# Kernel tuning notes

Measured on AMD Instinct MI355X. Metric: run time of the kernel, lower is better.

Reference implementation:

```python
import jax, jax.numpy as jnp
import numpy as np

N = 4096     # num nodes
FEAT = 500   # knn attribute dim
HID = 512    # args.hid_dim
E = 65536    # edges (avg degree 16)
T = 8        # args.time -> euler steps with step_size=1


def setup_inputs() -> dict:
    key = jax.random.key(0)
    ks = jax.random.split(key, 10)
    knn = jax.random.normal(ks[0], (N, FEAT), jnp.float32)
    adj = jax.random.uniform(ks[1], (N, N), jnp.float32)
    norm_factor = jnp.ones((), jnp.float32)
    edge_index = jax.random.randint(ks[2], (2, E), 0, N, dtype=jnp.int32).astype(jnp.int64)
    edge_weight = jax.random.uniform(ks[3], (E,), jnp.float32)
    # AGCN params (init eye + small noise so math is non-trivial)
    w1 = jnp.eye(N, dtype=jnp.float32) + 0.01 * jax.random.normal(ks[4], (N, N), jnp.float32)
    w2 = jnp.eye(N, dtype=jnp.float32) + 0.01 * jax.random.normal(ks[5], (N, N), jnp.float32)
    # extractor: Linear(N, HID) then Linear(HID, HID), kaiming-normal (relu), zero bias
    W0 = jax.random.normal(ks[6], (HID, N), jnp.float32) * np.float32((2.0 / N) ** 0.5)
    b0 = jnp.zeros((HID,), jnp.float32)
    W1 = jax.random.normal(ks[7], (HID, HID), jnp.float32) * np.float32((2.0 / HID) ** 0.5)
    b1 = jnp.zeros((HID,), jnp.float32)
    # LaplacianODEFunc scalar params
    alpha_train = jnp.asarray(0.5, jnp.float32)
    beta_train = jnp.asarray(0.1, jnp.float32)
    return dict(knn=knn, adj=adj, norm_factor=norm_factor, w1=w1, w2=w2,
                W0=W0, b0=b0, W1=W1, b1=b1, edge_weight=edge_weight,
                alpha_train=alpha_train, beta_train=beta_train, edge_index=edge_index)


def _spmm(edge_index, edge_weight, x):
    # out[row] += w * x[col], row=edge_index[0], col=edge_index[1]
    msg = edge_weight[:, None] * x[edge_index[1]]          # [E, HID]
    return jax.ops.segment_sum(msg, edge_index[0], num_segments=x.shape[0])


def reference(knn, adj, norm_factor, w1, w2, W0, b0, W1, b1,
              edge_weight, alpha_train, beta_train, edge_index):
    # ---- AGCN ----
    H = (adj @ w1) @ adj.T                                  # [N, N]
    H = (H @ w2) @ knn                                      # [N, FEAT]
    embed = H @ H.T                                         # [N, N]
    norm = jnp.maximum(jnp.linalg.norm(embed, axis=1, keepdims=True), 1e-12)
    embed = embed / norm                                    # F.normalize(dim=1)
    # ---- extractor MLP (no activation in source; dropout=eval no-op) ----
    h = embed @ W0.T + b0                                   # [N, HID]
    h = h @ W1.T + b1                                       # [N, HID]
    # ---- ODE diffusion: dx/dt = sigmoid(a)*(Ax - x) + b*x0, explicit Euler dt=1 ----
    x0 = jax.lax.stop_gradient(h)
    alpha = jax.nn.sigmoid(alpha_train)

    def step(x, _):
        ax = _spmm(edge_index, edge_weight, x)
        return x + alpha * (ax - x) + beta_train * x0, None

    z_ode, _ = jax.lax.scan(step, h, None, length=T)
    z = jax.nn.relu(norm_factor * z_ode + h)
    z = (z - z.mean(0)) / jnp.std(z, ddof=1)                # torch std is unbiased
    return z
```

## Files before the change

### kernel.cpp

```cpp
#include <hip/hip_runtime.h>
#include <stdint.h>
#include <stddef.h>

typedef __bf16 bf16;
typedef __attribute__((ext_vector_type(8))) __bf16 bf16x8;
typedef __attribute__((ext_vector_type(4))) __bf16 bf16x4;
typedef __attribute__((ext_vector_type(4))) float f32x4;

#define NN 4096
#define HIDD 512
#define NE 65536

__device__ inline void gll16(const void* g, void* l) {
    __builtin_amdgcn_global_load_lds(
        (const __attribute__((address_space(1))) void*)g,
        (__attribute__((address_space(3))) void*)l, 16, 0, 0);
}

__global__ void cvt8(const float* __restrict__ in, bf16* __restrict__ out, int n) {
    int i = (blockIdx.x * 256 + threadIdx.x) * 8;
    if (i >= n) return;
    float4 a = *reinterpret_cast<const float4*>(in + i);
    float4 b = *reinterpret_cast<const float4*>(in + i + 4);
    bf16x8 o;
    o[0] = (bf16)a.x; o[1] = (bf16)a.y; o[2] = (bf16)a.z; o[3] = (bf16)a.w;
    o[4] = (bf16)b.x; o[5] = (bf16)b.y; o[6] = (bf16)b.z; o[7] = (bf16)b.w;
    *reinterpret_cast<bf16x8*>(out + i) = o;
}

__global__ void reduce_bf16_slices(const bf16* __restrict__ in, bf16* __restrict__ out,
                                   int n, int S) {
    int i = (blockIdx.x * 256 + threadIdx.x) * 8;
    if (i >= n) return;
    float acc[8] = {};
    for (int k = 0; k < S; ++k) {
        bf16x8 v = *reinterpret_cast<const bf16x8*>(in + (size_t)k * n + i);
#pragma unroll
        for (int j = 0; j < 8; ++j) acc[j] += (float)v[j];
    }
    bf16x8 o;
#pragma unroll
    for (int j = 0; j < 8; ++j) o[j] = (bf16)acc[j];
    *reinterpret_cast<bf16x8*>(out + i) = o;
}

__global__ void transpose_pad_f32(const float* __restrict__ in, bf16* __restrict__ out,
                                  int R, int C, int Cpad) {
    __shared__ bf16 tile[32][33];
    int c0 = blockIdx.x * 32, r0 = blockIdx.y * 32;
    int tx = threadIdx.x, ty = threadIdx.y;
    for (int i = ty; i < 32; i += 8) {
        int r = r0 + i, c = c0 + tx;
        bf16 v = (bf16)0.f;
        if (r < R && c < C) v = (bf16)in[(size_t)r * C + c];
        tile[i][tx] = v;
    }
    __syncthreads();
    for (int i = ty; i < 32; i += 8) {
        int oc = c0 + i, orow = r0 + tx;
        if (oc < Cpad && orow < R) out[(size_t)oc * R + orow] = tile[tx][i];
    }
}

__global__ void transpose_dual_f32(const float* __restrict__ in, bf16* __restrict__ outT,
                                   bf16* __restrict__ outD, int Nn) {
    __shared__ bf16 tile[64][66];
    int r0 = blockIdx.y * 64, c0 = blockIdx.x * 64;
    int t = threadIdx.x;
    int cg = t & 7, rr = t >> 3;
#pragma unroll
    for (int i = 0; i < 2; ++i) {
        int r = rr + i * 32;
        const float* src = in + (size_t)(r0 + r) * Nn + c0 + cg * 8;
        float4 v0 = *reinterpret_cast<const float4*>(src);
        float4 v1 = *reinterpret_cast<const float4*>(src + 4);
        union { bf16x8 b; unsigned int u[4]; } cv;
        cv.b[0] = (bf16)v0.x; cv.b[1] = (bf16)v0.y; cv.b[2] = (bf16)v0.z; cv.b[3] = (bf16)v0.w;
        cv.b[4] = (bf16)v1.x; cv.b[5] = (bf16)v1.y; cv.b[6] = (bf16)v1.z; cv.b[7] = (bf16)v1.w;
        *reinterpret_cast<bf16x8*>(outD + (size_t)(r0 + r) * Nn + c0 + cg * 8) = cv.b;
        unsigned int* tw = reinterpret_cast<unsigned int*>(&tile[r][cg * 8]);
#pragma unroll
        for (int k = 0; k < 4; ++k) tw[k] = cv.u[k];
    }
    __syncthreads();
    int oc = t >> 3, rseg = (t & 7) * 8;
    bf16x8 w0, w1;
#pragma unroll
    for (int e = 0; e < 8; ++e) {
        w0[e] = tile[rseg + e][oc];
        w1[e] = tile[rseg + e][oc + 32];
    }
    *reinterpret_cast<bf16x8*>(outT + (size_t)(c0 + oc) * Nn + r0 + rseg) = w0;
    *reinterpret_cast<bf16x8*>(outT + (size_t)(c0 + oc + 32) * Nn + r0 + rseg) = w1;
}

__global__ void transpose_bf16(const bf16* __restrict__ in, bf16* __restrict__ out,
                               int R, int C) {
    __shared__ bf16 tile[32][33];
    int c0 = blockIdx.x * 32, r0 = blockIdx.y * 32;
    int tx = threadIdx.x, ty = threadIdx.y;
    for (int i = ty; i < 32; i += 8)
        tile[i][tx] = in[(size_t)(r0 + i) * C + c0 + tx];
    __syncthreads();
    for (int i = ty; i < 32; i += 8)
        out[(size_t)(c0 + i) * R + r0 + tx] = tile[tx][i];
}

template<int OMODE, bool HAS_BIAS, bool ROW_SCALE>
__global__ __launch_bounds__(256)
void gemm_nt(const bf16* __restrict__ A, const bf16* __restrict__ B,
             void* __restrict__ Cp, const float* __restrict__ bias,
             const float* __restrict__ rowscale, int M, int N, int K) {
    __shared__ __align__(16) bf16 As[3][128 * 32];
    __shared__ __align__(16) bf16 Bs[3][128 * 32];
    const int tid  = threadIdx.x;
    const int wave = tid >> 6;
    const int lane = tid & 63;
    const int m0 = blockIdx.y * 128, n0 = blockIdx.x * 128;
    const int lrow = lane >> 2;
    const int lcol = ((lane & 3) ^ ((lane >> 3) & 3)) * 8;
    const int c0 = wave * 2;
    const size_t arow0 = (size_t)(m0 + c0 * 16 + lrow) * K + lcol;
    const size_t arow1 = (size_t)(m0 + (c0 + 1) * 16 + lrow) * K + lcol;
    const size_t brow0 = (size_t)(n0 + c0 * 16 + lrow) * K + lcol;
    const size_t brow1 = (size_t)(n0 + (c0 + 1) * 16 + lrow) * K + lcol;

    f32x4 acc[4][4] = {};

    const int wm = (wave >> 1) * 64;
    const int wn = (wave & 1) * 64;
    const int fm = wm + (lane & 15);
    const int fn = wn + (lane & 15);
    const int fk = ((lane >> 4) ^ ((lane >> 1) & 3)) * 8;

    const int kper = K / gridDim.z;
    const int kz0 = blockIdx.z * kper;
    const int nt = kper >> 5;

    auto stage = [&](int t, int buf) {
        const int k0 = kz0 + (t << 5);
        gll16(A + arow0 + k0, &As[buf][c0 * 512]);
        gll16(A + arow1 + k0, &As[buf][(c0 + 1) * 512]);
        gll16(B + brow0 + k0, &Bs[buf][c0 * 512]);
        gll16(B + brow1 + k0, &Bs[buf][(c0 + 1) * 512]);
    };

    stage(0, 0);
    if (nt > 1) stage(1, 1);

    int cur = 0;
    for (int t = 0; t < nt; ++t) {
        if (t + 1 < nt) asm volatile("s_waitcnt vmcnt(4)" ::: "memory");
        else            asm volatile("s_waitcnt vmcnt(0)" ::: "memory");
        __builtin_amdgcn_s_barrier();
        if (t + 2 < nt) {
            int nb = cur + 2; if (nb >= 3) nb -= 3;
            stage(t + 2, nb);
        }
        bf16x8 af[4], bg[4];
#pragma unroll
        for (int i = 0; i < 4; ++i)
            af[i] = *reinterpret_cast<const bf16x8*>(&As[cur][(fm + i * 16) * 32 + fk]);
#pragma unroll
        for (int j = 0; j < 4; ++j)
            bg[j] = *reinterpret_cast<const bf16x8*>(&Bs[cur][(fn + j * 16) * 32 + fk]);
#pragma unroll
        for (int i = 0; i < 4; ++i)
#pragma unroll
            for (int j = 0; j < 4; ++j)
                acc[i][j] = __builtin_amdgcn_mfma_f32_16x16x32_bf16(af[i], bg[j], acc[i][j], 0, 0, 0);
        cur = (cur + 1 == 3) ? 0 : cur + 1;
    }

    const int rbase = m0 + wm + (lane >> 4) * 4;
    const int cbase = n0 + wn + (lane & 15);
    float* outf = (float*)Cp + (size_t)blockIdx.z * M * N;
    bf16*  outb = (bf16*)Cp;
    bf16*  outp = (bf16*)Cp + (size_t)blockIdx.z * M * N;
#pragma unroll
    for (int i = 0; i < 4; ++i) {
#pragma unroll
        for (int j = 0; j < 4; ++j) {
            int col = cbase + j * 16;
            float bv = 0.f;
            if (HAS_BIAS) bv = bias[col];
#pragma unroll
            for (int r = 0; r < 4; ++r) {
                int row = rbase + i * 16 + r;
                float v = acc[i][j][r];
                if (ROW_SCALE) v *= rowscale[row];
                v += bv;
                if (OMODE == 0)      outf[(size_t)row * N + col] = v;
                else if (OMODE == 1) outb[(size_t)row * N + col] = (bf16)v;
                else                 outp[(size_t)row * N + col] = (bf16)v;
            }
        }
    }
}

__global__ void colnorm_part(const bf16* __restrict__ Ht, const float* __restrict__ Rf,
                             float* __restrict__ n2) {
    int i = blockIdx.x * 128 + threadIdx.x;
    int a0 = blockIdx.y * 64;
    const size_t n = (size_t)HIDD * NN;
    float s = 0.f;
    for (int a = a0; a < a0 + 64; ++a) {
        size_t idx = (size_t)a * NN + i;
        float r = Rf[idx] + Rf[n + idx] + Rf[2 * n + idx] + Rf[3 * n + idx];
        s += r * (float)Ht[idx];
    }
    atomicAdd(&n2[i], s);
}

__global__ void bias_fuse(const float* __restrict__ W1, const float* __restrict__ b0,
                          const float* __restrict__ b1, float* __restrict__ bp) {
    int row = blockIdx.x * 4 + (threadIdx.x >> 6);
    int lane = threadIdx.x & 63;
    const float4* wr = (const float4*)(W1 + (size_t)row * HIDD);
    const float4* bz = (const float4*)b0;
    float s = 0.f;
#pragma unroll
    for (int j = 0; j < 2; ++j) {
        float4 a = wr[lane * 2 + j], b = bz[lane * 2 + j];
        s += a.x * b.x + a.y * b.y + a.z * b.z + a.w * b.w;
    }
    for (int off = 32; off; off >>= 1) s += __shfl_down(s, off);
    if (lane == 0) bp[row] = b1[row] + s;
}

__global__ void reduce4_scale_bias(const bf16* __restrict__ p, bf16* __restrict__ out,
                                   const float* __restrict__ n2, const float* __restrict__ bp) {
    int i = (blockIdx.x * 256 + threadIdx.x) * 8;
    const int n = NN * HIDD;
    float acc[8] = {};
#pragma unroll
    for (int s = 0; s < 4; ++s) {
        bf16x8 v = *reinterpret_cast<const bf16x8*>(p + (size_t)s * n + i);
#pragma unroll
        for (int j = 0; j < 8; ++j) acc[j] += (float)v[j];
    }
    int row = i >> 9;
    int col = i & (HIDD - 1);
    float sc = 1.f / fmaxf(sqrtf(n2[row]), 1e-12f);
    bf16x8 o;
#pragma unroll
    for (int j = 0; j < 8; ++j)
        o[j] = (bf16)(acc[j] * sc + bp[col + j]);
    *reinterpret_cast<bf16x8*>(out + i) = o;
}

__global__ void csr_count(const int* __restrict__ ei, int* __restrict__ cnt, int E) {
    int e = blockIdx.x * 256 + threadIdx.x;
    if (e < E) atomicAdd(&cnt[ei[e]], 1);
}

__global__ void scan_4096(const int* __restrict__ cnt, int* __restrict__ rs,
                          int* __restrict__ cur) {
    __shared__ int s[1024];
    int t = threadIdx.x;
    int b = t * 4;
    int a0 = cnt[b], a1 = cnt[b + 1], a2 = cnt[b + 2], a3 = cnt[b + 3];
    int tot = a0 + a1 + a2 + a3;
    s[t] = tot;
    __syncthreads();
    for (int off = 1; off < 1024; off <<= 1) {
        int v = (t >= off) ? s[t - off] : 0;
        __syncthreads();
        s[t] += v;
        __syncthreads();
    }
    int excl = s[t] - tot;
    rs[b] = excl; rs[b + 1] = excl + a0; rs[b + 2] = excl + a0 + a1; rs[b + 3] = excl + a0 + a1 + a2;
    cur[b] = excl; cur[b + 1] = excl + a0; cur[b + 2] = excl + a0 + a1; cur[b + 3] = excl + a0 + a1 + a2;
    if (t == 1023) rs[4096] = s[1023];
}

__global__ void csr_scatter(const int* __restrict__ ei, const float* __restrict__ ew,
                            int* __restrict__ cur, int* __restrict__ ccol,
                            float* __restrict__ cw, int E) {
    int e = blockIdx.x * 256 + threadIdx.x;
    if (e < E) {
        int r = ei[e];
        int p = atomicAdd(&cur[r], 1);
        ccol[p] = ei[E + e];
        cw[p] = ew[e];
    }
}

__global__ void ode_step_bf16(const bf16* __restrict__ xin, const bf16* __restrict__ x0,
                              bf16* __restrict__ xout, const int* __restrict__ rs,
                              const int* __restrict__ ccol, const float* __restrict__ cw,
                              const float* __restrict__ alpha_p, const float* __restrict__ beta_p) {
    int row = blockIdx.x * 4 + (threadIdx.x >> 6);
    int lane = threadIdx.x & 63;
    float alpha = 1.f / (1.f + expf(-alpha_p[0]));
    float beta = beta_p[0];
    const bf16x8* xin8 = (const bf16x8*)xin;
    float acc[8] = {};
    int p0 = rs[row], p1 = rs[row + 1];
    for (int p = p0; p < p1; ++p) {
        int c = ccol[p]; float w = cw[p];
        bf16x8 v = xin8[(size_t)c * 64 + lane];
#pragma unroll
        for (int j = 0; j < 8; ++j) acc[j] += w * (float)v[j];
    }
    bf16x8 xi = xin8[(size_t)row * 64 + lane];
    bf16x8 xz = ((const bf16x8*)x0)[(size_t)row * 64 + lane];
    bf16x8 r;
#pragma unroll
    for (int j = 0; j < 8; ++j) {
        float x = (float)xi[j];
        r[j] = (bf16)(x + alpha * (acc[j] - x) + beta * (float)xz[j]);
    }
    ((bf16x8*)xout)[(size_t)row * 64 + lane] = r;
}

__global__ void epi1(const bf16* __restrict__ x8, const bf16* __restrict__ h,
                     const float* __restrict__ nf_p,
                     float* __restrict__ colsum, float* __restrict__ gst) {
    __shared__ float r1[512], r2[512];
    int b = blockIdx.x, j = threadIdx.x;
    float nf = nf_p[0];
    float cp = 0.f, sq = 0.f;
    for (int i = 0; i < 8; ++i) {
        size_t idx = (size_t)(b * 8 + i) * HIDD + j;
        float v = nf * (float)x8[idx] + (float)h[idx];
        v = fmaxf(v, 0.f);
        cp += v; sq += v * v;
    }
    atomicAdd(&colsum[j], cp);
    r1[j] = cp; r2[j] = sq;
    __syncthreads();
    for (int off = 256; off > 0; off >>= 1) {
        if (j < off) { r1[j] += r1[j + off]; r2[j] += r2[j + off]; }
        __syncthreads();
    }
    if (j == 0) { atomicAdd(&gst[0], r1[0]); atomicAdd(&gst[1], r2[0]); }
}

__global__ void epi2(const bf16* __restrict__ x8, const bf16* __restrict__ h,
                     const float* __restrict__ nf_p, const float* __restrict__ colsum,
                     const float* __restrict__ gst, float* __restrict__ out) {
    int i = (blockIdx.x * 256 + threadIdx.x) * 8;
    float nf = nf_p[0];
    float n = (float)NN * (float)HIDD;
    float gmean = gst[0] / n;
    float var = (gst[1] - n * gmean * gmean) / (n - 1.f);
    float istd = rsqrtf(var);
    int col = i & (HIDD - 1);
    bf16x8 xv = *reinterpret_cast<const bf16x8*>(x8 + i);
    bf16x8 hv = *reinterpret_cast<const bf16x8*>(h + i);
    float4 o0, o1;
    float ov[8];
#pragma unroll
    for (int j = 0; j < 8; ++j) {
        float v = fmaxf(nf * (float)xv[j] + (float)hv[j], 0.f);
        float mean = colsum[col + j] * (1.f / (float)NN);
        ov[j] = (v - mean) * istd;
    }
    o0.x = ov[0]; o0.y = ov[1]; o0.z = ov[2]; o0.w = ov[3];
    o1.x = ov[4]; o1.y = ov[5]; o1.z = ov[6]; o1.w = ov[7];
    *reinterpret_cast<float4*>(out + i) = o0;
    *reinterpret_cast<float4*>(out + i + 4) = o1;
}

extern "C" void kernel_launch(void* const* d_in, const int* in_sizes, int n_in,
                              void* d_out, int out_size, void* d_ws, size_t ws_size,
                              hipStream_t stream) {
    const float* knn  = (const float*)d_in[0];
    const float* adj  = (const float*)d_in[1];
    const float* nf   = (const float*)d_in[2];
    const float* w1   = (const float*)d_in[3];
    const float* w2   = (const float*)d_in[4];
    const float* W0   = (const float*)d_in[5];
    const float* b0   = (const float*)d_in[6];
    const float* W1   = (const float*)d_in[7];
    const float* b1   = (const float*)d_in[8];
    const float* ew   = (const float*)d_in[9];
    const float* alph = (const float*)d_in[10];
    const float* beta = (const float*)d_in[11];
    const int*   ei   = (const int*)d_in[12];

    char* w = (char*)d_ws;
    size_t off = 0;
    auto alloc = [&](size_t bytes) -> char* {
        char* p = w + off;
        off += (bytes + 255) & ~(size_t)255;
        return p;
    };
    const size_t SZ_NN  = (size_t)NN * NN * sizeof(bf16);
    const size_t SZ_TH  = (size_t)HIDD * NN * sizeof(bf16);
    bf16* Bar  = (bf16*)alloc(SZ_NN);
    bf16* Car  = (bf16*)alloc(SZ_NN);
    bf16* Adjb = (bf16*)alloc(SZ_NN);
    bf16* W1big= (bf16*)alloc(SZ_NN);
    bf16* knnT = (bf16*)alloc(SZ_TH);
    bf16* tA   = (bf16*)alloc(SZ_TH);
    bf16* tB   = (bf16*)alloc(SZ_TH);
    float* tf  = (float*)alloc((size_t)32 * 1024 * 1024);
    bf16* Hm   = (bf16*)alloc(SZ_TH);
    bf16* W0b  = (bf16*)alloc(SZ_TH);
    bf16* W1sb = (bf16*)alloc((size_t)HIDD * HIDD * sizeof(bf16));
    bf16* Gb   = (bf16*)alloc((size_t)HIDD * HIDD * sizeof(bf16));
    bf16* M0b  = (bf16*)alloc((size_t)HIDD * HIDD * sizeof(bf16));
    bf16* Qtb  = (bf16*)alloc((size_t)HIDD * HIDD * sizeof(bf16));
    bf16* hb   = (bf16*)alloc((size_t)NN * HIDD * sizeof(bf16));
    float* n2  = (float*)alloc(NN * sizeof(float));
    int*  cnt  = (int*)alloc(NN * sizeof(int));
    int*  rs   = (int*)alloc((NN + 1) * sizeof(int));
    int*  cur  = (int*)alloc(NN * sizeof(int));
    int*  ccol = (int*)alloc(NE * sizeof(int));
    float* cw  = (float*)alloc(NE * sizeof(float));
    float* colsum = (float*)alloc(HIDD * sizeof(float));
    float* gst = (float*)alloc(2 * sizeof(float));
    float* bp  = (float*)alloc(HIDD * sizeof(float));
    bf16* tfb = (bf16*)tf;
    bf16* xA  = (bf16*)Car;
    bf16* xB  = (bf16*)Car + (size_t)NN * HIDD;
    (void)ws_size; (void)n_in; (void)in_sizes; (void)out_size;

    dim3 tb(32, 8);
    const int nTH = HIDD * NN;
    const int nHH = HIDD * HIDD;

    cvt8<<<(NN * NN) / 2048, 256, 0, stream>>>(w2, Car, NN * NN);
    cvt8<<<(NN * NN) / 2048, 256, 0, stream>>>(w1, W1big, NN * NN);
    cvt8<<<(HIDD * NN) / 2048, 256, 0, stream>>>(W0, W0b, HIDD * NN);
    cvt8<<<(HIDD * HIDD) / 2048, 256, 0, stream>>>(W1, W1sb, HIDD * HIDD);
    transpose_pad_f32<<<dim3(16, 128), tb, 0, stream>>>(knn, knnT, NN, 500, HIDD);
    transpose_dual_f32<<<dim3(64, 64), 256, 0, stream>>>(adj, Bar, Adjb, NN);

    gemm_nt<2, false, false><<<dim3(32, 4, 4), 256, 0, stream>>>(knnT, Car, tfb, nullptr, nullptr, HIDD, NN, NN);
    reduce_bf16_slices<<<nTH / 2048, 256, 0, stream>>>(tfb, tA, nTH, 4);
    gemm_nt<2, false, false><<<dim3(32, 4, 4), 256, 0, stream>>>(tA, Bar, tfb, nullptr, nullptr, HIDD, NN, NN);
    reduce_bf16_slices<<<nTH / 2048, 256, 0, stream>>>(tfb, tB, nTH, 4);
    gemm_nt<2, false, false><<<dim3(32, 4, 4), 256, 0, stream>>>(tB, W1big, tfb, nullptr, nullptr, HIDD, NN, NN);
    reduce_bf16_slices<<<nTH / 2048, 256, 0, stream>>>(tfb, tA, nTH, 4);
    gemm_nt<2, false, false><<<dim3(32, 4, 4), 256, 0, stream>>>(tA, Adjb, tfb, nullptr, nullptr, HIDD, NN, NN);
    reduce_bf16_slices<<<nTH / 2048, 256, 0, stream>>>(tfb, tB, nTH, 4);

    transpose_bf16<<<dim3(128, 16), tb, 0, stream>>>(tB, Hm, HIDD, NN);

    gemm_nt<2, false, false><<<dim3(4, 4, 32), 256, 0, stream>>>(tB, tB, tfb, nullptr, nullptr, HIDD, HIDD, NN);
    reduce_bf16_slices<<<nHH / 2048, 256, 0, stream>>>(tfb, Gb, nHH, 32);

    gemm_nt<0, false, false><<<dim3(32, 4, 4), 256, 0, stream>>>(Gb, Hm, tf, nullptr, nullptr, HIDD, NN, HIDD);
    hipMemsetAsync(n2, 0, NN * sizeof(float), stream);
    colnorm_part<<<dim3(32, 8), 128, 0, stream>>>(tB, tf, n2);

    gemm_nt<2, false, false><<<dim3(4, 4, 32), 256, 0, stream>>>(tB, W0b, tfb, nullptr, nullptr, HIDD, HIDD, NN);
    reduce_bf16_slices<<<nHH / 2048, 256, 0, stream>>>(tfb, M0b, nHH, 32);

    gemm_nt<2, false, false><<<dim3(4, 4, 8), 256, 0, stream>>>(W1sb, M0b, tfb, nullptr, nullptr, HIDD, HIDD, HIDD);
    reduce_bf16_slices<<<nHH / 2048, 256, 0, stream>>>(tfb, Qtb, nHH, 8);

    bias_fuse<<<128, 256, 0, stream>>>(W1, b0, b1, bp);

    gemm_nt<2, false, false><<<dim3(4, 32, 4), 256, 0, stream>>>(Hm, Qtb, tfb, nullptr, nullptr, NN, HIDD, HIDD);
    reduce4_scale_bias<<<(NN * HIDD) / 2048, 256, 0, stream>>>(tfb, hb, n2, bp);

    hipMemsetAsync(cnt, 0, NN * sizeof(int), stream);
    csr_count<<<NE / 256, 256, 0, stream>>>(ei, cnt, NE);
    scan_4096<<<1, 1024, 0, stream>>>(cnt, rs, cur);
    csr_scatter<<<NE / 256, 256, 0, stream>>>(ei, ew, cur, ccol, cw, NE);

    const bf16* xi = hb;
    bf16* xo = xA;
    for (int s = 0; s < 8; ++s) {
        ode_step_bf16<<<NN / 4, 256, 0, stream>>>(xi, hb, xo, rs, ccol, cw, alph, beta);
        xi = xo;
        xo = (s % 2 == 0) ? xB : xA;
    }

    hipMemsetAsync(colsum, 0, HIDD * sizeof(float), stream);
    hipMemsetAsync(gst, 0, 2 * sizeof(float), stream);
    epi1<<<NN / 8, 512, 0, stream>>>(xB, hb, nf, colsum, gst);
    epi2<<<(NN * HIDD) / 2048, 256, 0, stream>>>(xB, hb, nf, colsum, gst, (float*)d_out);
}
```

Measured before the change: 659.1 us.

## Remap GEMM blocks per XCD and halve split-K for the K=512 GEMMs

Adds an XCD-aware remapping of the flattened block index in the GEMM so blocks that are consecutive in the x/y/z order land on the same XCD, which should improve L2 reuse of the shared A/B tiles. Separately, the two K=512 GEMMs move from split-K of 4 to 2, with the colnorm and reduce kernels changed to sum two partial slices instead of four. This cuts partial-output traffic and reduction work, at the cost of fewer blocks and therefore lower occupancy in those GEMMs.

```diff
diff --git a/kernel.cpp b/kernel.cpp
--- a/kernel.cpp
+++ b/kernel.cpp
@@ -113,10 +113,21 @@
              const float* __restrict__ rowscale, int M, int N, int K) {
     __shared__ __align__(16) bf16 As[3][128 * 32];
     __shared__ __align__(16) bf16 Bs[3][128 * 32];
+    const int nx = gridDim.x, ny = gridDim.y, nz = gridDim.z;
+    const int total = nx * ny * nz;
+    int flat = blockIdx.x + nx * (blockIdx.y + ny * blockIdx.z);
+    int q = total >> 3, r8 = total & 7;
+    int xcd = flat & 7, idx = flat >> 3;
+    int swz = (xcd < r8 ? xcd * (q + 1) : r8 * (q + 1) + (xcd - r8) * q) + idx;
+    const int bx = swz / (ny * nz);
+    int rem = swz - bx * (ny * nz);
+    const int by = rem / nz;
+    const int bz = rem - by * nz;
+
     const int tid  = threadIdx.x;
     const int wave = tid >> 6;
     const int lane = tid & 63;
-    const int m0 = blockIdx.y * 128, n0 = blockIdx.x * 128;
+    const int m0 = by * 128, n0 = bx * 128;
     const int lrow = lane >> 2;
     const int lcol = ((lane & 3) ^ ((lane >> 3) & 3)) * 8;
     const int c0 = wave * 2;
@@ -133,8 +144,8 @@
     const int fn = wn + (lane & 15);
     const int fk = ((lane >> 4) ^ ((lane >> 1) & 3)) * 8;
 
-    const int kper = K / gridDim.z;
-    const int kz0 = blockIdx.z * kper;
+    const int kper = K / nz;
+    const int kz0 = bz * kper;
     const int nt = kper >> 5;
 
     auto stage = [&](int t, int buf) {
@@ -174,9 +185,9 @@
 
     const int rbase = m0 + wm + (lane >> 4) * 4;
     const int cbase = n0 + wn + (lane & 15);
-    float* outf = (float*)Cp + (size_t)blockIdx.z * M * N;
+    float* outf = (float*)Cp + (size_t)bz * M * N;
     bf16*  outb = (bf16*)Cp;
-    bf16*  outp = (bf16*)Cp + (size_t)blockIdx.z * M * N;
+    bf16*  outp = (bf16*)Cp + (size_t)bz * M * N;
 #pragma unroll
     for (int i = 0; i < 4; ++i) {
 #pragma unroll
@@ -202,12 +213,11 @@
                              float* __restrict__ n2) {
     int i = blockIdx.x * 128 + threadIdx.x;
     int a0 = blockIdx.y * 64;
-    const size_t n = (size_t)HIDD * NN;
+    const float* Rf2 = Rf + (size_t)HIDD * NN;
     float s = 0.f;
     for (int a = a0; a < a0 + 64; ++a) {
         size_t idx = (size_t)a * NN + i;
-        float r = Rf[idx] + Rf[n + idx] + Rf[2 * n + idx] + Rf[3 * n + idx];
-        s += r * (float)Ht[idx];
+        s += (Rf[idx] + Rf2[idx]) * (float)Ht[idx];
     }
     atomicAdd(&n2[i], s);
 }
@@ -228,24 +238,19 @@
     if (lane == 0) bp[row] = b1[row] + s;
 }
 
-__global__ void reduce4_scale_bias(const bf16* __restrict__ p, bf16* __restrict__ out,
+__global__ void reduce2_scale_bias(const bf16* __restrict__ p, bf16* __restrict__ out,
                                    const float* __restrict__ n2, const float* __restrict__ bp) {
     int i = (blockIdx.x * 256 + threadIdx.x) * 8;
     const int n = NN * HIDD;
-    float acc[8] = {};
-#pragma unroll
-    for (int s = 0; s < 4; ++s) {
-        bf16x8 v = *reinterpret_cast<const bf16x8*>(p + (size_t)s * n + i);
-#pragma unroll
-        for (int j = 0; j < 8; ++j) acc[j] += (float)v[j];
-    }
+    bf16x8 a = *reinterpret_cast<const bf16x8*>(p + i);
+    bf16x8 b = *reinterpret_cast<const bf16x8*>(p + n + i);
     int row = i >> 9;
     int col = i & (HIDD - 1);
     float sc = 1.f / fmaxf(sqrtf(n2[row]), 1e-12f);
     bf16x8 o;
 #pragma unroll
     for (int j = 0; j < 8; ++j)
-        o[j] = (bf16)(acc[j] * sc + bp[col + j]);
+        o[j] = (bf16)(((float)a[j] + (float)b[j]) * sc + bp[col + j]);
     *reinterpret_cast<bf16x8*>(out + i) = o;
 }
 
@@ -444,7 +449,7 @@
     gemm_nt<2, false, false><<<dim3(4, 4, 32), 256, 0, stream>>>(tB, tB, tfb, nullptr, nullptr, HIDD, HIDD, NN);
     reduce_bf16_slices<<<nHH / 2048, 256, 0, stream>>>(tfb, Gb, nHH, 32);
 
-    gemm_nt<0, false, false><<<dim3(32, 4, 4), 256, 0, stream>>>(Gb, Hm, tf, nullptr, nullptr, HIDD, NN, HIDD);
+    gemm_nt<0, false, false><<<dim3(32, 4, 2), 256, 0, stream>>>(Gb, Hm, tf, nullptr, nullptr, HIDD, NN, HIDD);
     hipMemsetAsync(n2, 0, NN * sizeof(float), stream);
     colnorm_part<<<dim3(32, 8), 128, 0, stream>>>(tB, tf, n2);
 
@@ -456,8 +461,8 @@
 
     bias_fuse<<<128, 256, 0, stream>>>(W1, b0, b1, bp);
 
-    gemm_nt<2, false, false><<<dim3(4, 32, 4), 256, 0, stream>>>(Hm, Qtb, tfb, nullptr, nullptr, NN, HIDD, HIDD);
-    reduce4_scale_bias<<<(NN * HIDD) / 2048, 256, 0, stream>>>(tfb, hb, n2, bp);
+    gemm_nt<2, false, false><<<dim3(4, 32, 2), 256, 0, stream>>>(Hm, Qtb, tfb, nullptr, nullptr, NN, HIDD, HIDD);
+    reduce2_scale_bias<<<(NN * HIDD) / 2048, 256, 0, stream>>>(tfb, hb, n2, bp);
 
     hipMemsetAsync(cnt, 0, NN * sizeof(int), stream);
     csr_count<<<NE / 256, 256, 0, stream>>>(ei, cnt, NE);
```

New measurement: 653.8 us. No clear change (-0.8%).

## Add 128x256 triple-buffered GEMM for big chain and trim split-K reductions

Applied to the files above, without the earlier changes.

Adds a new 512-thread GEMM kernel with 128x256 tiles, a three-stage LDS pipeline fed by global_load_lds and a swizzled layout. The four large 512x4096x4096 chain GEMMs use it with split-K of 8. Several smaller GEMMs drop from split-K 4 to 2, which lets the column-norm kernel run without atomics or a memset. The bias-fuse work is merged into the Q reduction kernel and the two epilogue memsets become one, cutting launch count. The risk is more split-K partial traffic in the big GEMMs and less parallelism in the shrunken splits.

```diff
diff --git a/kernel.cpp b/kernel.cpp
--- a/kernel.cpp
+++ b/kernel.cpp
@@ -198,54 +198,141 @@
     }
 }
 
-__global__ void colnorm_part(const bf16* __restrict__ Ht, const float* __restrict__ Rf,
-                             float* __restrict__ n2) {
+__global__ __launch_bounds__(512)
+void gemm_nt8(const bf16* __restrict__ A, const bf16* __restrict__ B,
+              void* __restrict__ Cp, int M, int N, int K) {
+    __shared__ __align__(16) bf16 As[3][128 * 32];
+    __shared__ __align__(16) bf16 Bs[3][256 * 32];
+    const int tid  = threadIdx.x;
+    const int wave = tid >> 6;
+    const int lane = tid & 63;
+    const int m0 = blockIdx.y * 128, n0 = blockIdx.x * 256;
+    const int lrow = lane >> 2;
+    const int lcol = ((lane & 3) ^ ((lane >> 3) & 3)) * 8;
+    const size_t arow  = (size_t)(m0 + wave * 16 + lrow) * K + lcol;
+    const size_t brow0 = (size_t)(n0 + wave * 32 + lrow) * K + lcol;
+    const size_t brow1 = (size_t)(n0 + wave * 32 + 16 + lrow) * K + lcol;
+
+    f32x4 acc[4][4] = {};
+
+    const int wm = (wave >> 2) * 64;
+    const int wn = (wave & 3) * 64;
+    const int fm = wm + (lane & 15);
+    const int fn = wn + (lane & 15);
+    const int fk = ((lane >> 4) ^ ((lane >> 1) & 3)) * 8;
+
+    const int kper = K / gridDim.z;
+    const int kz0 = blockIdx.z * kper;
+    const int nt = kper >> 5;
+
+    auto stage = [&](int t, int buf) {
+        const int k0 = kz0 + (t << 5);
+        gll16(A + arow  + k0, &As[buf][wave * 512]);
+        gll16(B + brow0 + k0, &Bs[buf][wave * 1024]);
+        gll16(B + brow1 + k0, &Bs[buf][wave * 1024 + 512]);
+    };
+
+    stage(0, 0);
+    if (nt > 1) stage(1, 1);
+
+    int cur = 0;
+    for (int t = 0; t < nt; ++t) {
+        if (t + 1 < nt) asm volatile("s_waitcnt vmcnt(3)" ::: "memory");
+        else            asm volatile("s_waitcnt vmcnt(0)" ::: "memory");
+        __builtin_amdgcn_s_barrier();
+        if (t + 2 < nt) {
+            int nb = cur + 2; if (nb >= 3) nb -= 3;
+            stage(t + 2, nb);
+        }
+        bf16x8 af[4], bg[4];
+#pragma unroll
+        for (int i = 0; i < 4; ++i)
+            af[i] = *reinterpret_cast<const bf16x8*>(&As[cur][(fm + i * 16) * 32 + fk]);
+#pragma unroll
+        for (int j = 0; j < 4; ++j)
+            bg[j] = *reinterpret_cast<const bf16x8*>(&Bs[cur][(fn + j * 16) * 32 + fk]);
+#pragma unroll
+        for (int i = 0; i < 4; ++i)
+#pragma unroll
+            for (int j = 0; j < 4; ++j)
+                acc[i][j] = __builtin_amdgcn_mfma_f32_16x16x32_bf16(af[i], bg[j], acc[i][j], 0, 0, 0);
+        cur = (cur + 1 == 3) ? 0 : cur + 1;
+    }
+
+    const int rbase = m0 + wm + (lane >> 4) * 4;
+    const int cbase = n0 + wn + (lane & 15);
+    bf16* outp = (bf16*)Cp + (size_t)blockIdx.z * M * N;
+#pragma unroll
+    for (int i = 0; i < 4; ++i) {
+#pragma unroll
+        for (int j = 0; j < 4; ++j) {
+            int col = cbase + j * 16;
+#pragma unroll
+            for (int r = 0; r < 4; ++r) {
+                int row = rbase + i * 16 + r;
+                outp[(size_t)row * N + col] = (bf16)acc[i][j][r];
+            }
+        }
+    }
+}
+
+__global__ void colnorm2(const bf16* __restrict__ Ht, const float* __restrict__ Rf,
+                         float* __restrict__ n2) {
     int i = blockIdx.x * 128 + threadIdx.x;
-    int a0 = blockIdx.y * 64;
-    const size_t n = (size_t)HIDD * NN;
+    const float* Rf2 = Rf + (size_t)HIDD * NN;
     float s = 0.f;
-    for (int a = a0; a < a0 + 64; ++a) {
+    for (int a = 0; a < HIDD; ++a) {
         size_t idx = (size_t)a * NN + i;
-        float r = Rf[idx] + Rf[n + idx] + Rf[2 * n + idx] + Rf[3 * n + idx];
-        s += r * (float)Ht[idx];
-    }
-    atomicAdd(&n2[i], s);
-}
-
-__global__ void bias_fuse(const float* __restrict__ W1, const float* __restrict__ b0,
-                          const float* __restrict__ b1, float* __restrict__ bp) {
-    int row = blockIdx.x * 4 + (threadIdx.x >> 6);
-    int lane = threadIdx.x & 63;
-    const float4* wr = (const float4*)(W1 + (size_t)row * HIDD);
-    const float4* bz = (const float4*)b0;
-    float s = 0.f;
-#pragma unroll
-    for (int j = 0; j < 2; ++j) {
-        float4 a = wr[lane * 2 + j], b = bz[lane * 2 + j];
-        s += a.x * b.x + a.y * b.y + a.z * b.z + a.w * b.w;
-    }
-    for (int off = 32; off; off >>= 1) s += __shfl_down(s, off);
-    if (lane == 0) bp[row] = b1[row] + s;
-}
-
-__global__ void reduce4_scale_bias(const bf16* __restrict__ p, bf16* __restrict__ out,
+        s += (Rf[idx] + Rf2[idx]) * (float)Ht[idx];
+    }
+    n2[i] = s;
+}
+
+__global__ void reduceQ_bias(const bf16* __restrict__ p, bf16* __restrict__ out, int n, int S,
+                             const float* __restrict__ W1, const float* __restrict__ b0,
+                             const float* __restrict__ b1, float* __restrict__ bp) {
+    if (blockIdx.x < 128) {
+        int i = (blockIdx.x * 256 + threadIdx.x) * 8;
+        if (i >= n) return;
+        float acc[8] = {};
+        for (int k = 0; k < S; ++k) {
+            bf16x8 v = *reinterpret_cast<const bf16x8*>(p + (size_t)k * n + i);
+#pragma unroll
+            for (int j = 0; j < 8; ++j) acc[j] += (float)v[j];
+        }
+        bf16x8 o;
+#pragma unroll
+        for (int j = 0; j < 8; ++j) o[j] = (bf16)acc[j];
+        *reinterpret_cast<bf16x8*>(out + i) = o;
+    } else {
+        int row = (blockIdx.x - 128) * 4 + (threadIdx.x >> 6);
+        int lane = threadIdx.x & 63;
+        const float4* wr = (const float4*)(W1 + (size_t)row * HIDD);
+        const float4* bz = (const float4*)b0;
+        float s = 0.f;
+#pragma unroll
+        for (int j = 0; j < 2; ++j) {
+            float4 a = wr[lane * 2 + j], b = bz[lane * 2 + j];
+            s += a.x * b.x + a.y * b.y + a.z * b.z + a.w * b.w;
+        }
+        for (int off = 32; off; off >>= 1) s += __shfl_down(s, off);
+        if (lane == 0) bp[row] = b1[row] + s;
+    }
+}
+
+__global__ void reduce2_scale_bias(const bf16* __restrict__ p, bf16* __restrict__ out,
                                    const float* __restrict__ n2, const float* __restrict__ bp) {
     int i = (blockIdx.x * 256 + threadIdx.x) * 8;
     const int n = NN * HIDD;
-    float acc[8] = {};
-#pragma unroll
-    for (int s = 0; s < 4; ++s) {
-        bf16x8 v = *reinterpret_cast<const bf16x8*>(p + (size_t)s * n + i);
-#pragma unroll
-        for (int j = 0; j < 8; ++j) acc[j] += (float)v[j];
-    }
+    bf16x8 a = *reinterpret_cast<const bf16x8*>(p + i);
+    bf16x8 b = *reinterpret_cast<const bf16x8*>(p + n + i);
     int row = i >> 9;
     int col = i & (HIDD - 1);
     float sc = 1.f / fmaxf(sqrtf(n2[row]), 1e-12f);
     bf16x8 o;
 #pragma unroll
     for (int j = 0; j < 8; ++j)
-        o[j] = (bf16)(acc[j] * sc + bp[col + j]);
+        o[j] = (bf16)(((float)a[j] + (float)b[j]) * sc + bp[col + j]);
     *reinterpret_cast<bf16x8*>(out + i) = o;
 }
 
@@ -411,8 +498,8 @@
     int*  cur  = (int*)alloc(NN * sizeof(int));
     int*  ccol = (int*)alloc(NE * sizeof(int));
     float* cw  = (float*)alloc(NE * sizeof(float));
-    float* colsum = (float*)alloc(HIDD * sizeof(float));
-    float* gst = (float*)alloc(2 * sizeof(float));
+    float* colsum = (float*)alloc(520 * sizeof(float));
+    float* gst = colsum + 512;
     float* bp  = (float*)alloc(HIDD * sizeof(float));
     bf16* tfb = (bf16*)tf;
     bf16* xA  = (bf16*)Car;
@@ -430,34 +517,31 @@
     transpose_pad_f32<<<dim3(16, 128), tb, 0, stream>>>(knn, knnT, NN, 500, HIDD);
     transpose_dual_f32<<<dim3(64, 64), 256, 0, stream>>>(adj, Bar, Adjb, NN);
 
-    gemm_nt<2, false, false><<<dim3(32, 4, 4), 256, 0, stream>>>(knnT, Car, tfb, nullptr, nullptr, HIDD, NN, NN);
-    reduce_bf16_slices<<<nTH / 2048, 256, 0, stream>>>(tfb, tA, nTH, 4);
-    gemm_nt<2, false, false><<<dim3(32, 4, 4), 256, 0, stream>>>(tA, Bar, tfb, nullptr, nullptr, HIDD, NN, NN);
-    reduce_bf16_slices<<<nTH / 2048, 256, 0, stream>>>(tfb, tB, nTH, 4);
-    gemm_nt<2, false, false><<<dim3(32, 4, 4), 256, 0, stream>>>(tB, W1big, tfb, nullptr, nullptr, HIDD, NN, NN);
-    reduce_bf16_slices<<<nTH / 2048, 256, 0, stream>>>(tfb, tA, nTH, 4);
-    gemm_nt<2, false, false><<<dim3(32, 4, 4), 256, 0, stream>>>(tA, Adjb, tfb, nullptr, nullptr, HIDD, NN, NN);
-    reduce_bf16_slices<<<nTH / 2048, 256, 0, stream>>>(tfb, tB, nTH, 4);
+    gemm_nt8<<<dim3(16, 4, 8), 512, 0, stream>>>(knnT, Car, tfb, HIDD, NN, NN);
+    reduce_bf16_slices<<<nTH / 2048, 256, 0, stream>>>(tfb, tA, nTH, 8);
+    gemm_nt8<<<dim3(16, 4, 8), 512, 0, stream>>>(tA, Bar, tfb, HIDD, NN, NN);
+    reduce_bf16_slices<<<nTH / 2048, 256, 0, stream>>>(tfb, tB, nTH, 8);
+    gemm_nt8<<<dim3(16, 4, 8), 512, 0, stream>>>(tB, W1big, tfb, HIDD, NN, NN);
+    reduce_bf16_slices<<<nTH / 2048, 256, 0, stream>>>(tfb, tA, nTH, 8);
+    gemm_nt8<<<dim3(16, 4, 8), 512, 0, stream>>>(tA, Adjb, tfb, HIDD, NN, NN);
+    reduce_bf16_slices<<<nTH / 2048, 256, 0, stream>>>(tfb, tB, nTH, 8);
 
     transpose_bf16<<<dim3(128, 16), tb, 0, stream>>>(tB, Hm, HIDD, NN);
 
     gemm_nt<2, false, false><<<dim3(4, 4, 32), 256, 0, stream>>>(tB, tB, tfb, nullptr, nullptr, HIDD, HIDD, NN);
     reduce_bf16_slices<<<nHH / 2048, 256, 0, stream>>>(tfb, Gb, nHH, 32);
 
-    gemm_nt<0, false, false><<<dim3(32, 4, 4), 256, 0, stream>>>(Gb, Hm, tf, nullptr, nullptr, HIDD, NN, HIDD);
-    hipMemsetAsync(n2, 0, NN * sizeof(float), stream);
-    colnorm_part<<<dim3(32, 8), 128, 0, stream>>>(tB, tf, n2);
+    gemm_nt<0, false, false><<<dim3(32, 4, 2), 256, 0, stream>>>(Gb, Hm, tf, nullptr, nullptr, HIDD, NN, HIDD);
+    colnorm2<<<32, 128, 0, stream>>>(tB, tf, n2);
 
     gemm_nt<2, false, false><<<dim3(4, 4, 32), 256, 0, stream>>>(tB, W0b, tfb, nullptr, nullptr, HIDD, HIDD, NN);
     reduce_bf16_slices<<<nHH / 2048, 256, 0, stream>>>(tfb, M0b, nHH, 32);
 
     gemm_nt<2, false, false><<<dim3(4, 4, 8), 256, 0, stream>>>(W1sb, M0b, tfb, nullptr, nullptr, HIDD, HIDD, HIDD);
-    reduce_bf16_slices<<<nHH / 2048, 256, 0, stream>>>(tfb, Qtb, nHH, 8);
-
-    bias_fuse<<<128, 256, 0, stream>>>(W1, b0, b1, bp);
-
-    gemm_nt<2, false, false><<<dim3(4, 32, 4), 256, 0, stream>>>(Hm, Qtb, tfb, nullptr, nullptr, NN, HIDD, HIDD);
-    reduce4_scale_bias<<<(NN * HIDD) / 2048, 256, 0, stream>>>(tfb, hb, n2, bp);
+    reduceQ_bias<<<256, 256, 0, stream>>>(tfb, Qtb, nHH, 8, W1, b0, b1, bp);
+
+    gemm_nt<2, false, false><<<dim3(4, 32, 2), 256, 0, stream>>>(Hm, Qtb, tfb, nullptr, nullptr, NN, HIDD, HIDD);
+    reduce2_scale_bias<<<(NN * HIDD) / 2048, 256, 0, stream>>>(tfb, hb, n2, bp);
 
     hipMemsetAsync(cnt, 0, NN * sizeof(int), stream);
     csr_count<<<NE / 256, 256, 0, stream>>>(ei, cnt, NE);
@@ -472,8 +556,7 @@
         xo = (s % 2 == 0) ? xB : xA;
     }
 
-    hipMemsetAsync(colsum, 0, HIDD * sizeof(float), stream);
-    hipMemsetAsync(gst, 0, 2 * sizeof(float), stream);
+    hipMemsetAsync(colsum, 0, 514 * sizeof(float), stream);
     epi1<<<NN / 8, 512, 0, stream>>>(xB, hb, nf, colsum, gst);
     epi2<<<(NN * HIDD) / 2048, 256, 0, stream>>>(xB, hb, nf, colsum, gst, (float*)d_out);
 }
```

Measured after the change: 673.5 us. 2.2% more time.
